# Kernel tuning notes

Hardware: AMD Instinct MI355X
Metric: run time of the kernel (lower is better)

Reference implementation:

```python
import jax, jax.numpy as jnp
import numpy as np

DIM, DSTATE, DCONV, DTRANK = 192, 16, 4, 12
BSZ, HH, WW = 2, 64, 64
DW = DIM * 2  # SGFN dw_dim


def _silu(x):
    return x * jax.nn.sigmoid(x)


def _mamba(u, in_w, conv_w, conv_b, xproj_w, dt_w, dt_b, A_log, Dp, out_w):
    # u: [B, L, d_model]; d_inner == d_model (expand=1)
    Bb, L, d = u.shape
    xz = jnp.einsum('bld,ed->ble', u, in_w)            # [B,L,2d]
    xm, z = jnp.split(xz, 2, axis=-1)
    # causal depthwise conv1d (pad left d_conv-1, truncate to L)
    xt = xm.transpose(0, 2, 1)                          # [B,d,L]
    xt = jax.lax.conv_general_dilated(
        xt, conv_w[:, None, :], (1,), [(DCONV - 1, 0)],
        feature_group_count=d, dimension_numbers=('NCH', 'OIH', 'NCH'))
    xm = _silu((xt + conv_b[:, None]).transpose(0, 2, 1))  # [B,L,d]
    x_dbl = jnp.einsum('bld,ed->ble', xm, xproj_w)      # [B,L,r+2N]
    dt, Bm, Cm = jnp.split(x_dbl, [DTRANK, DTRANK + DSTATE], axis=-1)
    dt = jax.nn.softplus(jnp.einsum('blr,dr->bld', dt, dt_w) + dt_b)  # [B,L,d]
    A = -jnp.exp(A_log)                                 # [d,N]
    dA = jnp.exp(dt[..., None] * A)                     # [B,L,d,N]
    dBu = dt[..., None] * Bm[:, :, None, :] * xm[..., None]  # [B,L,d,N]

    def step(h, inp):
        a, bu, c = inp
        h = a * h + bu                                  # [B,d,N]
        return h, jnp.einsum('bdn,bn->bd', h, c)

    h0 = jnp.zeros((Bb, d, DSTATE), u.dtype)
    _, ys = jax.lax.scan(step, h0, (dA.swapaxes(0, 1), dBu.swapaxes(0, 1), Cm.swapaxes(0, 1)))
    y = ys.swapaxes(0, 1) + Dp * xm                     # [B,L,d]
    y = y * _silu(z)
    return jnp.einsum('bld,ed->ble', y, out_w)


def _forward(x, ln_w, ln_b,
             in_w0, conv_w0, conv_b0, xproj_w0, dt_w0, dt_b0, A_log0, D0, out_w0,
             in_w1, conv_w1, conv_b1, xproj_w1, dt_w1, dt_b1, A_log1, D1, out_w1,
             scale_mod, c1w, c1b, dww, dwb, c2w, c2b, gamma):
    Bb, C, Hh, Wh = x.shape
    # LayerNorm over channel dim (applied in BHWC layout)
    xn = x.transpose(0, 2, 3, 1)
    mu = xn.mean(-1, keepdims=True)
    var = ((xn - mu) ** 2).mean(-1, keepdims=True)
    xn = (xn - mu) * jax.lax.rsqrt(var + 1e-5) * ln_w + ln_b
    # MHSS: bidirectional Mamba over flattened spatial sequence
    xf = xn.reshape(Bb, Hh * Wh, C)
    out = _mamba(xf, in_w0, conv_w0, conv_b0, xproj_w0, dt_w0, dt_b0, A_log0, D0, out_w0)
    out = out + _mamba(xf[:, ::-1], in_w1, conv_w1, conv_b1, xproj_w1, dt_w1, dt_b1, A_log1, D1, out_w1)[:, ::-1]
    xm = out.reshape(Bb, Hh, Wh, C).transpose(0, 3, 1, 2) * scale_mod
    # SGFN
    t = jnp.einsum('bchw,oc->bohw', xm, c1w) + c1b[:, None, None]
    t = jax.lax.conv_general_dilated(
        t, dww, (1, 1), [(1, 1), (1, 1)],
        feature_group_count=dww.shape[0],
        dimension_numbers=('NCHW', 'OIHW', 'NCHW')) + dwb[:, None, None]
    t1, t2 = jnp.split(t, 2, axis=1)
    sg = jnp.einsum('bchw,oc->bohw', t1 * jax.nn.sigmoid(t2), c2w) + c2b[:, None, None]
    return x + gamma * (xm + sg)


def _mamba_params(key):
    ks = jax.random.split(key, 6)
    d, s = DIM, 0.02
    dt = jnp.exp(jax.random.uniform(ks[4], (d,), minval=np.log(1e-3), maxval=np.log(1e-1)))
    return dict(
        in_w=jax.random.normal(ks[0], (2 * d, d)) * s,
        conv_w=jax.random.normal(ks[1], (d, DCONV)) * s,
        conv_b=jnp.zeros((d,)),
        xproj_w=jax.random.normal(ks[2], (DTRANK + 2 * DSTATE, d)) * s,
        dt_w=jax.random.normal(ks[3], (d, DTRANK)) * (DTRANK ** -0.5),
        dt_b=jnp.log(jnp.expm1(dt)),  # inverse softplus
        A_log=jnp.log(jnp.tile(jnp.arange(1, DSTATE + 1, dtype=jnp.float32), (d, 1))),
        D=jnp.ones((d,)),
        out_w=jax.random.normal(ks[5], (d, d)) * s,
    )


def setup_inputs() -> dict:
    key = jax.random.key(0)
    ks = jax.random.split(key, 8)
    p0 = _mamba_params(ks[1])
    p1 = _mamba_params(ks[2])
    s = 0.02
    inp = {
        'x': jax.random.normal(ks[0], (BSZ, DIM, HH, WW), jnp.float32),
        'ln_w': jnp.ones((DIM,)),
        'ln_b': jnp.zeros((DIM,)),
        'scale_mod': jnp.full((1,), 0.25),
        'c1w': jax.random.normal(ks[3], (2 * DW, DIM)) * s,
        'c1b': jnp.zeros((2 * DW,)),
        'dww': jax.random.normal(ks[4], (2 * DW, 1, 3, 3)) * s,
        'dwb': jnp.zeros((2 * DW,)),
        'c2w': jax.random.normal(ks[5], (DIM, DW)) * s,
        'c2b': jnp.zeros((DIM,)),
        'gamma': jnp.full((1,), 0.1),  # nonzero so the block is non-trivial
    }
    for name, p in (('0', p0), ('1', p1)):
        inp['in_w' + name] = p['in_w']
        inp['conv_w' + name] = p['conv_w']
        inp['conv_b' + name] = p['conv_b']
        inp['xproj_w' + name] = p['xproj_w']
        inp['dt_w' + name] = p['dt_w']
        inp['dt_b' + name] = p['dt_b']
        inp['A_log' + name] = p['A_log']
        inp['D' + name] = p['D']
        inp['out_w' + name] = p['out_w']
    return inp


def reference(x, ln_w, ln_b,
              in_w0, conv_w0, conv_b0, xproj_w0, dt_w0, dt_b0, A_log0, D0, out_w0,
              in_w1, conv_w1, conv_b1, xproj_w1, dt_w1, dt_b1, A_log1, D1, out_w1,
              scale_mod, c1w, c1b, dww, dwb, c2w, c2b, gamma):
    return _forward(x, ln_w, ln_b,
                    in_w0, conv_w0, conv_b0, xproj_w0, dt_w0, dt_b0, A_log0, D0, out_w0,
                    in_w1, conv_w1, conv_b1, xproj_w1, dt_w1, dt_b1, A_log1, D1, out_w1,
                    scale_mod, c1w, c1b, dww, dwb, c2w, c2b, gamma)
```

## Files before the change

### kernel.cpp

```cpp
#include <hip/hip_runtime.h>
#include <hip/hip_bf16.h>

#define BSZ   2
#define SEQL  4096
#define BLR   8192
#define DM    192
#define NST   16
#define DTR   12
#define XDW   44
#define XDP   48
#define NCH   128
#define CT    32

typedef float f32x4 __attribute__((ext_vector_type(4)));
typedef __bf16 bf16x8 __attribute__((ext_vector_type(8)));
typedef __bf16 bf16x4 __attribute__((ext_vector_type(4)));

__device__ __forceinline__ float sigf(float x) { return 1.f / (1.f + __expf(-x)); }
__device__ __forceinline__ float siluf(float x) { return x * sigf(x); }
__device__ __forceinline__ float softplusf(float x) { return x > 20.f ? x : log1pf(__expf(x)); }

#define PK_WIN  (768 * 192)
#define PK_WCT  (192 * 384)
#define PK_XPW  (2 * XDW * 192)
#define PK_C1W  (768 * 192)
#define PK_C2W  (192 * 384)
#define PK_DWT  (9 * 768)
#define PK_CWT  (4 * 384)
#define PK_CB   384
#define PK_TOT  (PK_WIN + PK_WCT + PK_XPW + PK_C1W + PK_C2W + PK_DWT + PK_CWT + PK_CB)
#define LN_BLOCKS 256
#define PK_BLOCKS ((PK_TOT + 255) / 256)

__global__ __launch_bounds__(256) void ln_pack_kernel(const float* __restrict__ x,
                                                      const float* __restrict__ lw,
                                                      const float* __restrict__ lb,
                                                      __bf16* __restrict__ xn,
                                                      const float* __restrict__ iw0, const float* __restrict__ iw1,
                                                      const float* __restrict__ ow0, const float* __restrict__ ow1,
                                                      const float* __restrict__ xp0, const float* __restrict__ xp1,
                                                      const float* __restrict__ c1w, const float* __restrict__ c2w,
                                                      const float* __restrict__ dww,
                                                      const float* __restrict__ cw0, const float* __restrict__ cw1,
                                                      const float* __restrict__ cb0, const float* __restrict__ cb1,
                                                      __bf16* __restrict__ win, __bf16* __restrict__ wcat,
                                                      __bf16* __restrict__ xpw, __bf16* __restrict__ c1wb,
                                                      __bf16* __restrict__ c2wb,
                                                      float* __restrict__ dwt, float* __restrict__ cwt,
                                                      float* __restrict__ cbc) {
    const int tid = threadIdx.x;
    if (blockIdx.x >= LN_BLOCKS) {
        int idx = (blockIdx.x - LN_BLOCKS) * 256 + tid;
        int base = 0;
        if (idx < base + PK_WIN) {
            int j = idx - base;
            win[j] = (__bf16)((j < 384 * 192) ? iw0[j] : iw1[j - 384 * 192]);
            return;
        }
        base += PK_WIN;
        if (idx < base + PK_WCT) {
            int j = idx - base;
            int n = j / 384, k = j % 384;
            wcat[j] = (__bf16)((k < DM) ? ow0[n * DM + k] : ow1[n * DM + k - DM]);
            return;
        }
        base += PK_WCT;
        if (idx < base + PK_XPW) {
            int j = idx - base;
            int dir = j / (XDW * 192);
            int rem = j - dir * (XDW * 192);
            int np = rem / 192, k = rem % 192;
            int src = (np < 32) ? (np + DTR) : (np - 32);
            xpw[j] = (__bf16)((dir ? xp1 : xp0)[src * 192 + k]);
            return;
        }
        base += PK_XPW;
        if (idx < base + PK_C1W) { c1wb[idx - base] = (__bf16)c1w[idx - base]; return; }
        base += PK_C1W;
        if (idx < base + PK_C2W) { c2wb[idx - base] = (__bf16)c2w[idx - base]; return; }
        base += PK_C2W;
        if (idx < base + PK_DWT) {
            int j = idx - base;
            int wi = j / 768, c = j % 768;
            dwt[j] = dww[c * 9 + wi];
            return;
        }
        base += PK_DWT;
        if (idx < base + PK_CWT) {
            int j = idx - base;
            int k = j / 384, col = j % 384;
            int dir = col >= DM, d = col - dir * DM;
            cwt[j] = (dir ? cw1 : cw0)[d * 4 + k];
            return;
        }
        base += PK_CWT;
        if (idx < base + PK_CB) {
            int col = idx - base;
            int dir = col >= DM, d = col - dir * DM;
            cbc[col] = (dir ? cb1 : cb0)[d];
        }
        return;
    }
    __shared__ float Xs[192][36];
    __shared__ float Rs[8][32], Rq[8][32];
    __shared__ float Mu[32], Rv[32];
    const int blk = blockIdx.x;
    const int b = blk >> 7;
    const int hw0 = (blk & 127) << 5;
    {
        int i4 = tid & 7, cp = tid >> 3;
        for (int c = cp; c < 192; c += 32) {
            float4 v = *reinterpret_cast<const float4*>(x + ((size_t)b * DM + c) * 4096 + hw0 + i4 * 4);
            *reinterpret_cast<float4*>(&Xs[c][i4 * 4]) = v;
        }
    }
    __syncthreads();
    const int i = tid & 31, part = tid >> 5;
    float s = 0.f, q = 0.f;
    for (int c = part * 24; c < part * 24 + 24; c++) {
        float v = Xs[c][i];
        s += v; q += v * v;
    }
    Rs[part][i] = s; Rq[part][i] = q;
    __syncthreads();
    if (part == 0) {
        float ss = 0.f, qq = 0.f;
#pragma unroll
        for (int p = 0; p < 8; p++) { ss += Rs[p][i]; qq += Rq[p][i]; }
        float mu = ss * (1.f / DM);
        float var = qq * (1.f / DM) - mu * mu;
        Mu[i] = mu; Rv[i] = rsqrtf(var + 1e-5f);
    }
    __syncthreads();
    float mu = Mu[i], rs = Rv[i];
    size_t rowb = ((size_t)b * 4096 + hw0 + i) * DM;
#pragma unroll
    for (int j = 0; j < 3; j++) {
        int c0 = part * 24 + j * 8;
        bf16x8 o;
#pragma unroll
        for (int e = 0; e < 8; e++) {
            int c = c0 + e;
            o[e] = (__bf16)((Xs[c][i] - mu) * rs * lw[c] + lb[c]);
        }
        *reinterpret_cast<bf16x8*>(xn + rowb + c0) = o;
    }
}

template <int EPI>
__global__ __launch_bounds__(256) void gemm_mfma(const __bf16* __restrict__ A, int lda,
                                                 const __bf16* __restrict__ W, int ldw,
                                                 __bf16* __restrict__ C, int ldc,
                                                 int N, int K,
                                                 const float* __restrict__ bias,
                                                 const float* __restrict__ scal,
                                                 const __bf16* __restrict__ aux,
                                                 const float* __restrict__ xres,
                                                 float* __restrict__ outp) {
    __shared__ __bf16 As[64][72];
    __shared__ __bf16 Ws[64][72];
    const int tid  = threadIdx.x;
    const int wave = tid >> 6, lane = tid & 63;
    const int ko = lane >> 4, lm = lane & 15;
    const int wm = (wave & 1) * 32, wn = (wave >> 1) * 32;
    const int m0 = blockIdx.y << 6;
    int n0 = blockIdx.x << 6;
    if (EPI == 5) {
        int dir = blockIdx.x;
        A += dir * DM;
        W += (size_t)dir * XDW * DM;
        C += (size_t)dir * BLR * XDP;
        n0 = 0;
    }
    const int r = tid >> 2, cq = (tid & 3) * 16;
    f32x4 acc[2][2] = {};

    for (int k0 = 0; k0 < K; k0 += 64) {
        {
            const __bf16* ap = A + (size_t)(m0 + r) * lda + k0 + cq;
            *reinterpret_cast<bf16x8*>(&As[r][cq])     = *reinterpret_cast<const bf16x8*>(ap);
            *reinterpret_cast<bf16x8*>(&As[r][cq + 8]) = *reinterpret_cast<const bf16x8*>(ap + 8);
        }
        {
            bf16x8 w0 = {}, w1 = {};
            if (n0 + r < N) {
                const __bf16* wp = W + (size_t)(n0 + r) * ldw + k0 + cq;
                w0 = *reinterpret_cast<const bf16x8*>(wp);
                w1 = *reinterpret_cast<const bf16x8*>(wp + 8);
            }
            *reinterpret_cast<bf16x8*>(&Ws[r][cq])     = w0;
            *reinterpret_cast<bf16x8*>(&Ws[r][cq + 8]) = w1;
        }
        __syncthreads();
#pragma unroll
        for (int kb = 0; kb < 2; kb++) {
            bf16x8 af[2], bfr[2];
#pragma unroll
            for (int ti = 0; ti < 2; ti++)
                af[ti] = *reinterpret_cast<bf16x8*>(&As[wm + ti * 16 + lm][kb * 32 + ko * 8]);
#pragma unroll
            for (int tj = 0; tj < 2; tj++)
                bfr[tj] = *reinterpret_cast<bf16x8*>(&Ws[wn + tj * 16 + lm][kb * 32 + ko * 8]);
#pragma unroll
            for (int ti = 0; ti < 2; ti++)
#pragma unroll
                for (int tj = 0; tj < 2; tj++)
                    acc[ti][tj] = __builtin_amdgcn_mfma_f32_16x16x32_bf16(af[ti], bfr[tj], acc[ti][tj], 0, 0, 0);
        }
        __syncthreads();
    }

    if constexpr (EPI == 4) {
        __shared__ float Cs[64][65];
#pragma unroll
        for (int ti = 0; ti < 2; ti++)
#pragma unroll
            for (int tj = 0; tj < 2; tj++) {
                int nn = n0 + wn + tj * 16 + lm;
#pragma unroll
                for (int reg = 0; reg < 4; reg++) {
                    int m = m0 + wm + ti * 16 + ko * 4 + reg;
                    float v = acc[ti][tj][reg];
                    if (nn < N) v += (float)aux[(size_t)m * DM + nn];
                    Cs[wm + ti * 16 + ko * 4 + reg][wn + tj * 16 + lm] = v;
                }
            }
        __syncthreads();
        float g = scal[0];
#pragma unroll
        for (int rep = 0; rep < 16; rep++) {
            int idx = rep * 256 + tid;
            int n = idx >> 6, mi = idx & 63;
            int nn = n0 + n;
            if (nn >= N) continue;
            int m = m0 + mi;
            int b = m >> 12, hw = m & 4095;
            size_t oi = (((size_t)b * DM + nn) << 12) + hw;
            outp[oi] = xres[oi] + g * (Cs[mi][n] + bias[nn]);
        }
        return;
    }

#pragma unroll
    for (int ti = 0; ti < 2; ti++)
#pragma unroll
        for (int tj = 0; tj < 2; tj++) {
            int n = n0 + wn + tj * 16 + lm;
            if (n >= N) continue;
#pragma unroll
            for (int reg = 0; reg < 4; reg++) {
                int m = m0 + wm + ti * 16 + ko * 4 + reg;
                float v = acc[ti][tj][reg];
                if (EPI == 1) v += bias[n];
                if (EPI == 3) v *= scal[0];
                C[(size_t)m * ldc + n] = (__bf16)v;
            }
        }
}

__global__ __launch_bounds__(256) void conv_silu_kernel(const __bf16* __restrict__ xz,
                                                        const float* __restrict__ cwt,
                                                        const float* __restrict__ cbcat,
                                                        __bf16* __restrict__ xc) {
    int idx = blockIdx.x * 256 + threadIdx.x;
    int colq = (idx % 48) << 3;
    int row = idx / 48;
    int dir = colq >= DM;
    int b = row >> 12, l = row & 4095;
    int xoff = colq + dir * DM;
    float acc[8];
    {
        float4 b0 = *reinterpret_cast<const float4*>(cbcat + colq);
        float4 b1 = *reinterpret_cast<const float4*>(cbcat + colq + 4);
        acc[0] = b0.x; acc[1] = b0.y; acc[2] = b0.z; acc[3] = b0.w;
        acc[4] = b1.x; acc[5] = b1.y; acc[6] = b1.z; acc[7] = b1.w;
    }
#pragma unroll
    for (int k = 0; k < 4; k++) {
        int ls = dir ? (l + 3 - k) : (l - 3 + k);
        if (ls < 0 || ls >= SEQL) continue;
        bf16x8 xv = *reinterpret_cast<const bf16x8*>(xz + ((size_t)(b << 12) + ls) * 768 + xoff);
        const float* wv = cwt + k * 384 + colq;
#pragma unroll
        for (int e = 0; e < 8; e++) acc[e] += wv[e] * (float)xv[e];
    }
    bf16x8 o;
#pragma unroll
    for (int e = 0; e < 8; e++) o[e] = (__bf16)siluf(acc[e]);
    *reinterpret_cast<bf16x8*>(xc + (size_t)row * 384 + colq) = o;
}

__global__ __launch_bounds__(384) void scan_partial(const __bf16* __restrict__ xcb,
                                                    const __bf16* __restrict__ xd,
                                                    const float* __restrict__ dtw0,
                                                    const float* __restrict__ dtw1,
                                                    const float* __restrict__ dtb0,
                                                    const float* __restrict__ dtb1,
                                                    const float* __restrict__ Alog0,
                                                    const float* __restrict__ Alog1,
                                                    float* __restrict__ S, float* __restrict__ P) {
    int tid = threadIdx.x;
    int d = tid >> 1, half = tid & 1;
    int blk = blockIdx.x;
    int chunk = blk & (NCH - 1);
    int dirb = blk >> 7;
    int b = dirb >> 1, dir = dirb & 1;
    const float* Alog = dir ? Alog1 : Alog0;
    const float* dtw  = dir ? dtw1 : dtw0;
    float dtb = (dir ? dtb1 : dtb0)[d];
    float wdt[12];
#pragma unroll
    for (int r = 0; r < 12; r++) wdt[r] = dtw[d * DTR + r];
    float A[8], h[8];
#pragma unroll
    for (int n = 0; n < 8; n++) { A[n] = -__expf(Alog[d * NST + half * 8 + n]); h[n] = 0.f; }
    float sdt = 0.f;
    int col = dir * DM + d;
    const __bf16* xdd = xd + (size_t)dir * BLR * XDP;
    int l0 = chunk * CT;
    for (int s = 0; s < CT; s++) {
        int l = dir ? (SEQL - 1 - (l0 + s)) : (l0 + s);
        size_t row = ((size_t)b << 12) + l;
        const __bf16* xr = xdd + row * XDP;
        bf16x8 Bv = *reinterpret_cast<const bf16x8*>(xr + half * 8);
        bf16x8 R0 = *reinterpret_cast<const bf16x8*>(xr + 32);
        bf16x4 R1 = *reinterpret_cast<const bf16x4*>(xr + 40);
        float dtraw = dtb;
#pragma unroll
        for (int r = 0; r < 8; r++) dtraw += wdt[r] * (float)R0[r];
#pragma unroll
        for (int r = 0; r < 4; r++) dtraw += wdt[8 + r] * (float)R1[r];
        float dtv = softplusf(dtraw);
        float xcv = (float)xcb[row * 384 + col];
        float dx = dtv * xcv;
#pragma unroll
        for (int n = 0; n < 8; n++)
            h[n] = __expf(dtv * A[n]) * h[n] + dx * (float)Bv[n];
        sdt += dtv;
    }
    float* Sp = S + (size_t)blk * 3072 + d * 16 + half * 8;
    float* Pp = P + (size_t)blk * 3072 + d * 16 + half * 8;
#pragma unroll
    for (int q = 0; q < 2; q++) {
        *reinterpret_cast<float4*>(Sp + q * 4) =
            make_float4(h[q * 4], h[q * 4 + 1], h[q * 4 + 2], h[q * 4 + 3]);
        *reinterpret_cast<float4*>(Pp + q * 4) =
            make_float4(__expf(A[q * 4] * sdt), __expf(A[q * 4 + 1] * sdt),
                        __expf(A[q * 4 + 2] * sdt), __expf(A[q * 4 + 3] * sdt));
    }
}

__global__ __launch_bounds__(256) void scan_combine(float* SH, const float* __restrict__ P) {
    int id = blockIdx.x * 256 + threadIdx.x;
    int dirb = id / 3072;
    int dn = id % 3072;
    float h = 0.f;
#pragma unroll 4
    for (int c = 0; c < NCH; c++) {
        size_t idx = (size_t)(dirb * NCH + c) * 3072 + dn;
        float s = SH[idx], p = P[idx];
        SH[idx] = h;
        h = p * h + s;
    }
}

__global__ __launch_bounds__(384) void scan_apply(const __bf16* __restrict__ xcb,
                                                  const __bf16* __restrict__ xd,
                                                  const __bf16* __restrict__ xzb,
                                                  const float* __restrict__ dtw0,
                                                  const float* __restrict__ dtw1,
                                                  const float* __restrict__ dtb0,
                                                  const float* __restrict__ dtb1,
                                                  const float* __restrict__ Alog0,
                                                  const float* __restrict__ Alog1,
                                                  const float* __restrict__ D0,
                                                  const float* __restrict__ D1,
                                                  const float* __restrict__ Hini,
                                                  __bf16* __restrict__ y) {
    int tid = threadIdx.x;
    int d = tid >> 1, half = tid & 1;
    int blk = blockIdx.x;
    int chunk = blk & (NCH - 1);
    int dirb = blk >> 7;
    int b = dirb >> 1, dir = dirb & 1;
    const float* Alog = dir ? Alog1 : Alog0;
    const float* dtw  = dir ? dtw1 : dtw0;
    float dtb = (dir ? dtb1 : dtb0)[d];
    float Dv = (dir ? D1 : D0)[d];
    float wdt[12];
#pragma unroll
    for (int r = 0; r < 12; r++) wdt[r] = dtw[d * DTR + r];
    float A[8], h[8];
#pragma unroll
    for (int n = 0; n < 8; n++) A[n] = -__expf(Alog[d * NST + half * 8 + n]);
    {
        const float* Hp = Hini + (size_t)blk * 3072 + d * 16 + half * 8;
        float4 h0 = *reinterpret_cast<const float4*>(Hp);
        float4 h1 = *reinterpret_cast<const float4*>(Hp + 4);
        h[0] = h0.x; h[1] = h0.y; h[2] = h0.z; h[3] = h0.w;
        h[4] = h1.x; h[5] = h1.y; h[6] = h1.z; h[7] = h1.w;
    }
    int col = dir * DM + d;
    const __bf16* xdd = xd + (size_t)dir * BLR * XDP;
    int l0 = chunk * CT;
    for (int s = 0; s < CT; s++) {
        int l = dir ? (SEQL - 1 - (l0 + s)) : (l0 + s);
        size_t row = ((size_t)b << 12) + l;
        const __bf16* xr = xdd + row * XDP;
        bf16x8 Bv = *reinterpret_cast<const bf16x8*>(xr + half * 8);
        bf16x8 Cv = *reinterpret_cast<const bf16x8*>(xr + 16 + half * 8);
        bf16x8 R0 = *reinterpret_cast<const bf16x8*>(xr + 32);
        bf16x4 R1 = *reinterpret_cast<const bf16x4*>(xr + 40);
        float dtraw = dtb;
#pragma unroll
        for (int r = 0; r < 8; r++) dtraw += wdt[r] * (float)R0[r];
#pragma unroll
        for (int r = 0; r < 4; r++) dtraw += wdt[8 + r] * (float)R1[r];
        float dtv = softplusf(dtraw);
        float xcv = (float)xcb[row * 384 + col];
        float dx = dtv * xcv;
        float p = 0.f;
#pragma unroll
        for (int n = 0; n < 8; n++) {
            h[n] = __expf(dtv * A[n]) * h[n] + dx * (float)Bv[n];
            p += h[n] * (float)Cv[n];
        }
        p += __shfl_xor(p, 1);
        if (half == 0) {
            float zv = (float)xzb[row * 768 + dir * 384 + DM + d];
            y[row * 384 + col] = (__bf16)((p + Dv * xcv) * siluf(zv));
        }
    }
}

__global__ __launch_bounds__(256) void dwgate_kernel(const __bf16* __restrict__ t,
                                                     const float* __restrict__ dwt,
                                                     const float* __restrict__ dwb,
                                                     __bf16* __restrict__ g) {
    int idx = blockIdx.x * 256 + threadIdx.x;
    int jq = (idx % 48) << 3;
    int row = idx / 48;
    int b = row >> 12, hw = row & 4095;
    int h = hw >> 6, w = hw & 63;
    float a1[8], a2[8];
    {
        float4 x0 = *reinterpret_cast<const float4*>(dwb + jq);
        float4 x1 = *reinterpret_cast<const float4*>(dwb + jq + 4);
        float4 y0 = *reinterpret_cast<const float4*>(dwb + 384 + jq);
        float4 y1 = *reinterpret_cast<const float4*>(dwb + 384 + jq + 4);
        a1[0]=x0.x;a1[1]=x0.y;a1[2]=x0.z;a1[3]=x0.w;a1[4]=x1.x;a1[5]=x1.y;a1[6]=x1.z;a1[7]=x1.w;
        a2[0]=y0.x;a2[1]=y0.y;a2[2]=y0.z;a2[3]=y0.w;a2[4]=y1.x;a2[5]=y1.y;a2[6]=y1.z;a2[7]=y1.w;
    }
#pragma unroll
    for (int dy = -1; dy <= 1; dy++) {
        int hh = h + dy;
        if (hh < 0 || hh >= 64) continue;
#pragma unroll
        for (int dx = -1; dx <= 1; dx++) {
            int ww = w + dx;
            if (ww < 0 || ww >= 64) continue;
            size_t base = ((size_t)(b << 12) + (hh << 6) + ww) * 768;
            int wi = (dy + 1) * 3 + (dx + 1);
            bf16x8 t1 = *reinterpret_cast<const bf16x8*>(t + base + jq);
            bf16x8 t2 = *reinterpret_cast<const bf16x8*>(t + base + 384 + jq);
            const float* w1 = dwt + wi * 768 + jq;
            const float* w2 = dwt + wi * 768 + 384 + jq;
#pragma unroll
            for (int e = 0; e < 8; e++) {
                a1[e] += w1[e] * (float)t1[e];
                a2[e] += w2[e] * (float)t2[e];
            }
        }
    }
    bf16x8 o;
#pragma unroll
    for (int e = 0; e < 8; e++) o[e] = (__bf16)(a1[e] * sigf(a2[e]));
    *reinterpret_cast<bf16x8*>(g + (size_t)row * 384 + jq) = o;
}

extern "C" void kernel_launch(void* const* d_in, const int* in_sizes, int n_in,
                              void* d_out, int out_size, void* d_ws, size_t ws_size,
                              hipStream_t stream) {
    const float* x         = (const float*)d_in[0];
    const float* ln_w      = (const float*)d_in[1];
    const float* ln_b      = (const float*)d_in[2];
    const float* scale_mod = (const float*)d_in[3];
    const float* c1w       = (const float*)d_in[4];
    const float* c1b       = (const float*)d_in[5];
    const float* dww       = (const float*)d_in[6];
    const float* dwb       = (const float*)d_in[7];
    const float* c2w       = (const float*)d_in[8];
    const float* c2b       = (const float*)d_in[9];
    const float* gamma     = (const float*)d_in[10];
    const float* in_w0     = (const float*)d_in[11];
    const float* conv_w0   = (const float*)d_in[12];
    const float* conv_b0   = (const float*)d_in[13];
    const float* xproj_w0  = (const float*)d_in[14];
    const float* dt_w0     = (const float*)d_in[15];
    const float* dt_b0     = (const float*)d_in[16];
    const float* A_log0    = (const float*)d_in[17];
    const float* D0        = (const float*)d_in[18];
    const float* out_w0    = (const float*)d_in[19];
    const float* in_w1     = (const float*)d_in[20];
    const float* conv_w1   = (const float*)d_in[21];
    const float* conv_b1   = (const float*)d_in[22];
    const float* xproj_w1  = (const float*)d_in[23];
    const float* dt_w1     = (const float*)d_in[24];
    const float* dt_b1     = (const float*)d_in[25];
    const float* A_log1    = (const float*)d_in[26];
    const float* D1        = (const float*)d_in[27];
    const float* out_w1    = (const float*)d_in[28];

    char* wsb = (char*)d_ws;
    size_t off = 0;
    auto alloc = [&](size_t bytes) { size_t o = off; off += (bytes + 255) & ~(size_t)255; return o; };
    const size_t o_xn   = alloc((size_t)BLR * DM * 2);
    const size_t o_xz   = alloc((size_t)BLR * 768 * 2);
    const size_t o_xc   = alloc((size_t)BLR * 384 * 2);
    const size_t o_y    = alloc((size_t)BLR * 384 * 2);
    const size_t o_xm   = alloc((size_t)BLR * DM * 2);
    const size_t o_xd   = alloc((size_t)2 * BLR * XDP * 2);
    const size_t o_S    = alloc((size_t)4 * NCH * 3072 * 4);
    const size_t o_P    = alloc((size_t)4 * NCH * 3072 * 4);
    const size_t o_win  = alloc((size_t)PK_WIN * 2);
    const size_t o_wct  = alloc((size_t)PK_WCT * 2);
    const size_t o_xpw  = alloc((size_t)PK_XPW * 2);
    const size_t o_c1w  = alloc((size_t)PK_C1W * 2);
    const size_t o_c2w  = alloc((size_t)PK_C2W * 2);
    const size_t o_dwt  = alloc((size_t)PK_DWT * 4);
    const size_t o_cwt  = alloc((size_t)PK_CWT * 4);
    const size_t o_cb   = alloc((size_t)PK_CB * 4);

    __bf16* xn  = (__bf16*)(wsb + o_xn);
    __bf16* xz  = (__bf16*)(wsb + o_xz);
    __bf16* xc  = (__bf16*)(wsb + o_xc);
    __bf16* yb  = (__bf16*)(wsb + o_y);
    __bf16* xm  = (__bf16*)(wsb + o_xm);
    __bf16* xd  = (__bf16*)(wsb + o_xd);
    float*  Sb  = (float*)(wsb + o_S);
    float*  Pb  = (float*)(wsb + o_P);
    __bf16* win = (__bf16*)(wsb + o_win);
    __bf16* wct = (__bf16*)(wsb + o_wct);
    __bf16* xpw = (__bf16*)(wsb + o_xpw);
    __bf16* c1wb= (__bf16*)(wsb + o_c1w);
    __bf16* c2wb= (__bf16*)(wsb + o_c2w);
    float*  dwt = (float*)(wsb + o_dwt);
    float*  cwt = (float*)(wsb + o_cwt);
    float*  cbc = (float*)(wsb + o_cb);

    ln_pack_kernel<<<LN_BLOCKS + PK_BLOCKS, 256, 0, stream>>>(
        x, ln_w, ln_b, xn,
        in_w0, in_w1, out_w0, out_w1, xproj_w0, xproj_w1, c1w, c2w,
        dww, conv_w0, conv_w1, conv_b0, conv_b1,
        win, wct, xpw, c1wb, c2wb, dwt, cwt, cbc);
    gemm_mfma<0><<<dim3(12, 128), 256, 0, stream>>>(xn, DM, win, DM, xz, 768, 768, DM,
                                                    nullptr, nullptr, nullptr, nullptr, nullptr);
    conv_silu_kernel<<<(BLR * 48) / 256, 256, 0, stream>>>(xz, cwt, cbc, xc);
    gemm_mfma<5><<<dim3(2, 128), 256, 0, stream>>>(xc, 384, xpw, DM, xd, XDP, XDW, DM,
                                                   nullptr, nullptr, nullptr, nullptr, nullptr);
    scan_partial<<<4 * NCH, 384, 0, stream>>>(xc, xd, dt_w0, dt_w1, dt_b0, dt_b1,
                                              A_log0, A_log1, Sb, Pb);
    scan_combine<<<48, 256, 0, stream>>>(Sb, Pb);
    scan_apply<<<4 * NCH, 384, 0, stream>>>(xc, xd, xz, dt_w0, dt_w1, dt_b0, dt_b1,
                                            A_log0, A_log1, D0, D1, Sb, yb);
    gemm_mfma<3><<<dim3(3, 128), 256, 0, stream>>>(yb, 384, wct, 384, xm, DM, DM, 384,
                                                   nullptr, scale_mod, nullptr, nullptr, nullptr);
    gemm_mfma<1><<<dim3(12, 128), 256, 0, stream>>>(xm, DM, c1wb, DM, xz, 768, 768, DM,
                                                    c1b, nullptr, nullptr, nullptr, nullptr);
    dwgate_kernel<<<(BLR * 48) / 256, 256, 0, stream>>>(xz, dwt, dwb, xc);
    gemm_mfma<4><<<dim3(3, 128), 256, 0, stream>>>(xc, 384, c2wb, 384, nullptr, 0, DM, 384,
                                                   c2b, gamma, xm, x, (float*)d_out);
}
```

Measured before the change: 306.5 us.

## Give each scan thread all 16 states and double the chunk count

Remaps the chunked selective-scan kernels so each thread owns one channel with all 16 state entries, instead of two threads splitting 8 states each. This drops the cross-lane shuffle and removes the duplicated dt projection and softplus work that both halves used to compute. To keep parallelism, the chunk count doubles and the chunk length halves, and the block size halves. The combine pass now walks twice as many chunks, and the partial-state buffers double in size, which adds serial work and memory traffic there. Register use per thread also rises.

```diff
diff --git a/kernel.cpp b/kernel.cpp
--- a/kernel.cpp
+++ b/kernel.cpp
@@ -9,8 +9,8 @@
 #define DTR   12
 #define XDW   44
 #define XDP   48
-#define NCH   128
-#define CT    32
+#define NCH   256
+#define CT    16
 
 typedef float f32x4 __attribute__((ext_vector_type(4)));
 typedef __bf16 bf16x8 __attribute__((ext_vector_type(8)));
@@ -290,7 +290,7 @@
     *reinterpret_cast<bf16x8*>(xc + (size_t)row * 384 + colq) = o;
 }
 
-__global__ __launch_bounds__(384) void scan_partial(const __bf16* __restrict__ xcb,
+__global__ __launch_bounds__(192) void scan_partial(const __bf16* __restrict__ xcb,
                                                     const __bf16* __restrict__ xd,
                                                     const float* __restrict__ dtw0,
                                                     const float* __restrict__ dtw1,
@@ -299,11 +299,10 @@
                                                     const float* __restrict__ Alog0,
                                                     const float* __restrict__ Alog1,
                                                     float* __restrict__ S, float* __restrict__ P) {
-    int tid = threadIdx.x;
-    int d = tid >> 1, half = tid & 1;
+    int d = threadIdx.x;
     int blk = blockIdx.x;
     int chunk = blk & (NCH - 1);
-    int dirb = blk >> 7;
+    int dirb = blk >> 8;
     int b = dirb >> 1, dir = dirb & 1;
     const float* Alog = dir ? Alog1 : Alog0;
     const float* dtw  = dir ? dtw1 : dtw0;
@@ -311,18 +310,20 @@
     float wdt[12];
 #pragma unroll
     for (int r = 0; r < 12; r++) wdt[r] = dtw[d * DTR + r];
-    float A[8], h[8];
-#pragma unroll
-    for (int n = 0; n < 8; n++) { A[n] = -__expf(Alog[d * NST + half * 8 + n]); h[n] = 0.f; }
+    float A[16], h[16];
+#pragma unroll
+    for (int n = 0; n < 16; n++) { A[n] = -__expf(Alog[d * NST + n]); h[n] = 0.f; }
     float sdt = 0.f;
     int col = dir * DM + d;
     const __bf16* xdd = xd + (size_t)dir * BLR * XDP;
     int l0 = chunk * CT;
+#pragma unroll 2
     for (int s = 0; s < CT; s++) {
         int l = dir ? (SEQL - 1 - (l0 + s)) : (l0 + s);
         size_t row = ((size_t)b << 12) + l;
         const __bf16* xr = xdd + row * XDP;
-        bf16x8 Bv = *reinterpret_cast<const bf16x8*>(xr + half * 8);
+        bf16x8 B0 = *reinterpret_cast<const bf16x8*>(xr);
+        bf16x8 B1 = *reinterpret_cast<const bf16x8*>(xr + 8);
         bf16x8 R0 = *reinterpret_cast<const bf16x8*>(xr + 32);
         bf16x4 R1 = *reinterpret_cast<const bf16x4*>(xr + 40);
         float dtraw = dtb;
@@ -334,19 +335,19 @@
         float xcv = (float)xcb[row * 384 + col];
         float dx = dtv * xcv;
 #pragma unroll
-        for (int n = 0; n < 8; n++)
-            h[n] = __expf(dtv * A[n]) * h[n] + dx * (float)Bv[n];
+        for (int n = 0; n < 16; n++) {
+            float Bv = (float)(n < 8 ? B0[n & 7] : B1[n & 7]);
+            h[n] = __expf(dtv * A[n]) * h[n] + dx * Bv;
+        }
         sdt += dtv;
     }
-    float* Sp = S + (size_t)blk * 3072 + d * 16 + half * 8;
-    float* Pp = P + (size_t)blk * 3072 + d * 16 + half * 8;
-#pragma unroll
-    for (int q = 0; q < 2; q++) {
-        *reinterpret_cast<float4*>(Sp + q * 4) =
-            make_float4(h[q * 4], h[q * 4 + 1], h[q * 4 + 2], h[q * 4 + 3]);
-        *reinterpret_cast<float4*>(Pp + q * 4) =
-            make_float4(__expf(A[q * 4] * sdt), __expf(A[q * 4 + 1] * sdt),
-                        __expf(A[q * 4 + 2] * sdt), __expf(A[q * 4 + 3] * sdt));
+    float4* Sp = reinterpret_cast<float4*>(S + (size_t)blk * 3072 + d * 16);
+    float4* Pp = reinterpret_cast<float4*>(P + (size_t)blk * 3072 + d * 16);
+#pragma unroll
+    for (int q = 0; q < 4; q++) {
+        Sp[q] = make_float4(h[q * 4], h[q * 4 + 1], h[q * 4 + 2], h[q * 4 + 3]);
+        Pp[q] = make_float4(__expf(A[q * 4] * sdt), __expf(A[q * 4 + 1] * sdt),
+                            __expf(A[q * 4 + 2] * sdt), __expf(A[q * 4 + 3] * sdt));
     }
 }
 
@@ -364,7 +365,7 @@
     }
 }
 
-__global__ __launch_bounds__(384) void scan_apply(const __bf16* __restrict__ xcb,
+__global__ __launch_bounds__(192) void scan_apply(const __bf16* __restrict__ xcb,
                                                   const __bf16* __restrict__ xd,
                                                   const __bf16* __restrict__ xzb,
                                                   const float* __restrict__ dtw0,
@@ -377,11 +378,10 @@
                                                   const float* __restrict__ D1,
                                                   const float* __restrict__ Hini,
                                                   __bf16* __restrict__ y) {
-    int tid = threadIdx.x;
-    int d = tid >> 1, half = tid & 1;
+    int d = threadIdx.x;
     int blk = blockIdx.x;
     int chunk = blk & (NCH - 1);
-    int dirb = blk >> 7;
+    int dirb = blk >> 8;
     int b = dirb >> 1, dir = dirb & 1;
     const float* Alog = dir ? Alog1 : Alog0;
     const float* dtw  = dir ? dtw1 : dtw0;
@@ -390,25 +390,27 @@
     float wdt[12];
 #pragma unroll
     for (int r = 0; r < 12; r++) wdt[r] = dtw[d * DTR + r];
-    float A[8], h[8];
-#pragma unroll
-    for (int n = 0; n < 8; n++) A[n] = -__expf(Alog[d * NST + half * 8 + n]);
-    {
-        const float* Hp = Hini + (size_t)blk * 3072 + d * 16 + half * 8;
-        float4 h0 = *reinterpret_cast<const float4*>(Hp);
-        float4 h1 = *reinterpret_cast<const float4*>(Hp + 4);
-        h[0] = h0.x; h[1] = h0.y; h[2] = h0.z; h[3] = h0.w;
-        h[4] = h1.x; h[5] = h1.y; h[6] = h1.z; h[7] = h1.w;
+    float A[16], h[16];
+#pragma unroll
+    for (int n = 0; n < 16; n++) A[n] = -__expf(Alog[d * NST + n]);
+    const float4* Hp = reinterpret_cast<const float4*>(Hini + (size_t)blk * 3072 + d * 16);
+#pragma unroll
+    for (int q = 0; q < 4; q++) {
+        float4 hq = Hp[q];
+        h[q * 4] = hq.x; h[q * 4 + 1] = hq.y; h[q * 4 + 2] = hq.z; h[q * 4 + 3] = hq.w;
     }
     int col = dir * DM + d;
     const __bf16* xdd = xd + (size_t)dir * BLR * XDP;
     int l0 = chunk * CT;
+#pragma unroll 2
     for (int s = 0; s < CT; s++) {
         int l = dir ? (SEQL - 1 - (l0 + s)) : (l0 + s);
         size_t row = ((size_t)b << 12) + l;
         const __bf16* xr = xdd + row * XDP;
-        bf16x8 Bv = *reinterpret_cast<const bf16x8*>(xr + half * 8);
-        bf16x8 Cv = *reinterpret_cast<const bf16x8*>(xr + 16 + half * 8);
+        bf16x8 B0 = *reinterpret_cast<const bf16x8*>(xr);
+        bf16x8 B1 = *reinterpret_cast<const bf16x8*>(xr + 8);
+        bf16x8 C0 = *reinterpret_cast<const bf16x8*>(xr + 16);
+        bf16x8 C1 = *reinterpret_cast<const bf16x8*>(xr + 24);
         bf16x8 R0 = *reinterpret_cast<const bf16x8*>(xr + 32);
         bf16x4 R1 = *reinterpret_cast<const bf16x4*>(xr + 40);
         float dtraw = dtb;
@@ -421,15 +423,14 @@
         float dx = dtv * xcv;
         float p = 0.f;
 #pragma unroll
-        for (int n = 0; n < 8; n++) {
-            h[n] = __expf(dtv * A[n]) * h[n] + dx * (float)Bv[n];
-            p += h[n] * (float)Cv[n];
-        }
-        p += __shfl_xor(p, 1);
-        if (half == 0) {
-            float zv = (float)xzb[row * 768 + dir * 384 + DM + d];
-            y[row * 384 + col] = (__bf16)((p + Dv * xcv) * siluf(zv));
-        }
+        for (int n = 0; n < 16; n++) {
+            float Bv = (float)(n < 8 ? B0[n & 7] : B1[n & 7]);
+            float Cv = (float)(n < 8 ? C0[n & 7] : C1[n & 7]);
+            h[n] = __expf(dtv * A[n]) * h[n] + dx * Bv;
+            p += h[n] * Cv;
+        }
+        float zv = (float)xzb[row * 768 + dir * 384 + DM + d];
+        y[row * 384 + col] = (__bf16)((p + Dv * xcv) * siluf(zv));
     }
 }
 
@@ -558,10 +559,10 @@
     conv_silu_kernel<<<(BLR * 48) / 256, 256, 0, stream>>>(xz, cwt, cbc, xc);
     gemm_mfma<5><<<dim3(2, 128), 256, 0, stream>>>(xc, 384, xpw, DM, xd, XDP, XDW, DM,
                                                    nullptr, nullptr, nullptr, nullptr, nullptr);
-    scan_partial<<<4 * NCH, 384, 0, stream>>>(xc, xd, dt_w0, dt_w1, dt_b0, dt_b1,
+    scan_partial<<<4 * NCH, 192, 0, stream>>>(xc, xd, dt_w0, dt_w1, dt_b0, dt_b1,
                                               A_log0, A_log1, Sb, Pb);
     scan_combine<<<48, 256, 0, stream>>>(Sb, Pb);
-    scan_apply<<<4 * NCH, 384, 0, stream>>>(xc, xd, xz, dt_w0, dt_w1, dt_b0, dt_b1,
+    scan_apply<<<4 * NCH, 192, 0, stream>>>(xc, xd, xz, dt_w0, dt_w1, dt_b0, dt_b1,
                                             A_log0, A_log1, D0, D1, Sb, yb);
     gemm_mfma<3><<<dim3(3, 128), 256, 0, stream>>>(yb, 384, wct, 384, xm, DM, DM, 384,
                                                    nullptr, scale_mod, nullptr, nullptr, nullptr);
```

Result: faster. 279.7 us (-8.7%).
